# Kernel tuning notes

Hardware: AMD Instinct MI355X
Metric: run time of the kernel (lower is better)

The kernel has to match this reference:

```python
import jax, jax.numpy as jnp
import numpy as np

H = 768      # hidden_size
R = 16       # num_relations
NS = 64      # num_support
NQ = 128     # num_query
STEPS = 3    # propagation_steps


def setup_inputs() -> dict:
    key = jax.random.key(0)
    ks = jax.random.split(key, 16)
    s_h = 1.0 / np.sqrt(H)
    s_2h = 1.0 / np.sqrt(2 * H)
    f32 = jnp.float32
    return {
        'aspect_embeddings': jax.random.normal(ks[0], (NS, H), f32),
        'query_embeddings': jax.random.normal(ks[1], (NQ, H), f32),
        'support_labels': jax.random.randint(ks[2], (NS,), 0, 5),
        # similarity network: Linear(2H->H), ReLU, Linear(H->R), Softmax
        'W1s': (jax.random.normal(ks[3], (H, 2 * H), f32) * s_2h),
        'b1s': jnp.zeros((H,), f32),
        'W2s': (jax.random.normal(ks[4], (R, H), f32) * s_h),
        'b2s': jnp.zeros((R,), f32),
        # diversity network
        'W1d': (jax.random.normal(ks[5], (H, 2 * H), f32) * s_2h),
        'b1d': jnp.zeros((H,), f32),
        'W2d': (jax.random.normal(ks[6], (R, H), f32) * s_h),
        'b2d': jnp.zeros((R,), f32),
        # relation matrices [R, H, H] (scaled for numerical stability)
        'Rs': (jax.random.normal(ks[7], (R, H, H), f32) * s_h),
        'Rd': (jax.random.normal(ks[8], (R, H, H), f32) * s_h),
        # message MLP: Linear(H->H), ReLU, Linear(H->H)
        'Wm1': (jax.random.normal(ks[9], (H, H), f32) * s_h),
        'bm1': jnp.zeros((H,), f32),
        'Wm2': (jax.random.normal(ks[10], (H, H), f32) * s_h),
        'bm2': jnp.zeros((H,), f32),
        # GRUCell params (gate order: r, z, n as in torch)
        'Wih': (jax.random.normal(ks[11], (3 * H, H), f32) * s_h),
        'Whh': (jax.random.normal(ks[12], (3 * H, H), f32) * s_h),
        'bih': jnp.zeros((3 * H,), f32),
        'bhh': jnp.zeros((3 * H,), f32),
    }


def _relation_net(pf, W1, b1, W2, b2):
    # pf: [N, N, 2H] -> softmax weights [N, N, R]; dropout is identity (eval)
    hid = jax.nn.relu(jnp.einsum('ijk,hk->ijh', pf, W1) + b1)
    return jax.nn.softmax(jnp.einsum('ijh,rh->ijr', hid, W2) + b2, axis=-1)


def _drp_forward(aspect_embeddings, query_embeddings,
                 W1s, b1s, W2s, b2s, W1d, b1d, W2d, b2d,
                 Rs, Rd, Wm1, bm1, Wm2, bm2, Wih, Whh, bih, bhh):
    h = jnp.concatenate([aspect_embeddings, query_embeddings], axis=0)  # [N, H]
    N = h.shape[0]
    for _ in range(STEPS):
        # pairwise features [N, N, 2H]: (node_i, node_j)
        pf = jnp.concatenate([
            jnp.broadcast_to(h[:, None, :], (N, N, H)),
            jnp.broadcast_to(h[None, :, :], (N, N, H)),
        ], axis=-1)
        sw = _relation_net(pf, W1s, b1s, W2s, b2s)  # [N, N, R]
        dw = _relation_net(pf, W1d, b1d, W2d, b2d)  # [N, N, R]
        # relation-transformed embeddings: [N, R, H]
        ts = jnp.einsum('jh,rhd->jrd', h, Rs)
        td = jnp.einsum('jh,rhd->jrd', h, Rd)
        # relation-weighted messages: [N, N, H]
        msgs = jnp.einsum('ijr,jrd->ijd', sw, ts) + jnp.einsum('ijr,jrd->ijd', dw, td)
        pm = jax.nn.relu(msgs @ Wm1.T + bm1) @ Wm2.T + bm2  # [N, N, H]
        x = pm.mean(axis=1)  # aggregated message per node [N, H]
        # GRUCell update (torch gate order r, z, n)
        gx = x @ Wih.T + bih
        gh = h @ Whh.T + bhh
        r = jax.nn.sigmoid(gx[:, :H] + gh[:, :H])
        z = jax.nn.sigmoid(gx[:, H:2 * H] + gh[:, H:2 * H])
        n = jnp.tanh(gx[:, 2 * H:] + r * gh[:, 2 * H:])
        h = (1.0 - z) * n + z * h
    return h[NS:]  # updated query embeddings [NQ, H]


def reference(aspect_embeddings, support_labels, query_embeddings,
              W1s, b1s, W2s, b2s, W1d, b1d, W2d, b2d,
              Rs, Rd, Wm1, bm1, Wm2, bm2, Wih, Whh, bih, bhh):
    # support_labels is unused in the original forward
    return _drp_forward(aspect_embeddings, query_embeddings,
                        W1s, b1s, W2s, b2s, W1d, b1d, W2d, b2d,
                        Rs, Rd, Wm1, bm1, Wm2, bm2, Wih, Whh, bih, bhh)
```

## Files before the change

### kernel.cpp

```cpp
#include <hip/hip_runtime.h>
#include <hip/hip_bf16.h>

#define H 768
#define NTOT 192
#define A4W 3072
#define GW 2304

typedef __attribute__((ext_vector_type(4))) float f32x4;
typedef __attribute__((ext_vector_type(8))) unsigned short u16x8;
typedef __attribute__((ext_vector_type(4))) unsigned short u16x4;
typedef __attribute__((ext_vector_type(8))) __bf16 bf16x8v;

static __device__ __forceinline__ unsigned short f2bf(float f) {
  __hip_bfloat16 b = __float2bfloat16(f);
  return __builtin_bit_cast(unsigned short, b);
}
static __device__ __forceinline__ float bf2f(unsigned short u) {
  return __bfloat162float(__builtin_bit_cast(__hip_bfloat16, u));
}
static __device__ __forceinline__ f32x4 MFMA(u16x8 a, u16x8 b, f32x4 c) {
  return __builtin_amdgcn_mfma_f32_16x16x32_bf16(
      __builtin_bit_cast(bf16x8v, a), __builtin_bit_cast(bf16x8v, b), c, 0, 0, 0);
}
static __device__ __forceinline__ u16x8 ld8(const unsigned short* p) {
  return *(const u16x8*)p;
}
static __device__ __forceinline__ unsigned int cvtpk(float lo, float hi) {
  unsigned int r;
  asm("v_cvt_pk_bf16_f32 %0, %1, %2" : "=v"(r) : "v"(lo), "v"(hi));
  return r;
}
static __device__ __forceinline__ float relu(float x) { return fmaxf(x, 0.f); }

#define GLDS16(gp, lp)                                                   \
  __builtin_amdgcn_global_load_lds(                                      \
      (const __attribute__((address_space(1))) void*)(gp),               \
      (__attribute__((address_space(3))) void*)(lp), 16, 0, 0)

__global__ void k_prep(const float* __restrict__ Wm1, const float* __restrict__ W2s,
                       const float* __restrict__ W2d, const float* __restrict__ Whh,
                       const float* __restrict__ Wih, const float* __restrict__ Wm2,
                       const float* __restrict__ W1s, const float* __restrict__ W1d,
                       const float* __restrict__ b1s, const float* __restrict__ b1d,
                       const float* __restrict__ bm2, const float* __restrict__ bih,
                       const float* __restrict__ asp, const float* __restrict__ qry,
                       unsigned short* __restrict__ Wm1bf, unsigned short* __restrict__ W2sbf,
                       unsigned short* __restrict__ W2dbf, unsigned short* __restrict__ Whhh,
                       unsigned short* __restrict__ Whhl, unsigned short* __restrict__ Wm2th,
                       unsigned short* __restrict__ Wm2tl, unsigned short* __restrict__ W1cat,
                       float* __restrict__ b1cat, float* __restrict__ bc,
                       float* __restrict__ h, unsigned short* __restrict__ hhi,
                       unsigned short* __restrict__ hlo) {
  const int b = blockIdx.x, tid = threadIdx.x;
  if (b < 576) {
    int u = b * 256 + tid;
    float4 v = ((const float4*)Wm1)[u];
    u16x4 o; o[0] = f2bf(v.x); o[1] = f2bf(v.y); o[2] = f2bf(v.z); o[3] = f2bf(v.w);
    ((u16x4*)Wm1bf)[u] = o;
  } else if (b < 588) {
    int u = (b - 576) * 256 + tid;
    float4 v = ((const float4*)W2s)[u];
    u16x4 o; o[0] = f2bf(v.x); o[1] = f2bf(v.y); o[2] = f2bf(v.z); o[3] = f2bf(v.w);
    ((u16x4*)W2sbf)[u] = o;
  } else if (b < 600) {
    int u = (b - 588) * 256 + tid;
    float4 v = ((const float4*)W2d)[u];
    u16x4 o; o[0] = f2bf(v.x); o[1] = f2bf(v.y); o[2] = f2bf(v.z); o[3] = f2bf(v.w);
    ((u16x4*)W2dbf)[u] = o;
  } else if (b < 2328) {
    int u = (b - 600) * 256 + tid;
    float4 v = ((const float4*)Whh)[u];
    u16x4 oh, ol;
#pragma unroll
    for (int j = 0; j < 4; ++j) {
      float f = ((const float*)&v)[j];
      oh[j] = f2bf(f); ol[j] = f2bf(f - bf2f(oh[j]));
    }
    ((u16x4*)Whhh)[u] = oh; ((u16x4*)Whhl)[u] = ol;
  } else if (b < 2904) {
    int u = (b - 2328) * 256 + tid;
    float4 v = ((const float4*)Wm2)[u];
    int e_lin = u * 4;
    int er = e_lin / H, kc = e_lin - er * H;
#pragma unroll
    for (int j = 0; j < 4; ++j) {
      float f = ((const float*)&v)[j];
      unsigned short hi = f2bf(f);
      Wm2th[(size_t)(kc + j) * H + er] = hi;
      Wm2tl[(size_t)(kc + j) * H + er] = f2bf(f - bf2f(hi));
    }
  } else if (b < 5208) {
    int u = (b - 2904) * 256 + tid;
    int e = u * 4;
    int row = e / H, k = e - row * H;
    int part = row / H, o = row - part * H;
    const float* W = (part < 2) ? W1s : W1d;
    float4 v = *(const float4*)(W + (size_t)o * (2 * H) + (part & 1) * H + k);
    u16x4 ov; ov[0] = f2bf(v.x); ov[1] = f2bf(v.y); ov[2] = f2bf(v.z); ov[3] = f2bf(v.w);
    *(u16x4*)(W1cat + e) = ov;
    if (u < 768) {
      int e2 = u * 4, pp = e2 / H, oo = e2 - pp * H;
      float4 bv;
      if (pp == 0) bv = *(const float4*)(b1s + oo);
      else if (pp == 2) bv = *(const float4*)(b1d + oo);
      else bv = (float4){0.f, 0.f, 0.f, 0.f};
      *(float4*)(b1cat + e2) = bv;
    }
  } else if (b < 5784) {
    const int w = tid >> 6, l = tid & 63;
    const int gg = (b - 5208) * 4 + w;
    const float* row = Wih + (size_t)gg * H;
    float s = 0.f;
#pragma unroll
    for (int q = 0; q < 12; ++q) s += row[l + q * 64] * bm2[l + q * 64];
#pragma unroll
    for (int m = 32; m; m >>= 1) s += __shfl_xor(s, m);
    if (l == 0) bc[gg] = bih[gg] + s;
  } else {
    int u = (b - 5784) * 256 + tid;
    float4 v = (u < 12288) ? ((const float4*)asp)[u] : ((const float4*)qry)[u - 12288];
    ((float4*)h)[u] = v;
    u16x4 oh, ol;
#pragma unroll
    for (int j = 0; j < 4; ++j) {
      float f = ((const float*)&v)[j];
      oh[j] = f2bf(f); ol[j] = f2bf(f - bf2f(oh[j]));
    }
    ((u16x4*)hhi)[u] = oh; ((u16x4*)hlo)[u] = ol;
  }
}

__global__ __launch_bounds__(256) void k_pre2(const unsigned short* __restrict__ Wm1bf,
                                              const float* __restrict__ Rsf,
                                              const float* __restrict__ Rdf,
                                              unsigned short* __restrict__ RsWt,
                                              const float* __restrict__ Wih,
                                              const unsigned short* __restrict__ Bth,
                                              const unsigned short* __restrict__ Btl,
                                              unsigned short* __restrict__ Ch,
                                              unsigned short* __restrict__ Cl) {
  __shared__ unsigned short LDS[16384];
  const int wg = blockIdx.x;
  const int tid = threadIdx.x, w = tid >> 6, l = tid & 63;
  const int g = l >> 4, ln = l & 15;
  const int srow = l >> 3;
  const int skb = ((l & 7) ^ srow) * 8;
  const int x7 = ln & 7;

  if (wg >= 1152) {
    unsigned short* Ahl = LDS;
    unsigned short* All = LDS + 4096;
    unsigned short* Bhl = LDS + 8192;
    unsigned short* Bll = LDS + 12288;
    const int bid = wg - 1152;
    const int m0 = (bid / 12) * 64, n0 = (bid % 12) * 64;
    const unsigned short* Bgh = Bth + (size_t)(n0 + srow) * H + skb;
    const unsigned short* Bgl = Btl + (size_t)(n0 + srow) * H + skb;
    f32x4 acc[4];
#pragma unroll
    for (int mi = 0; mi < 4; ++mi) acc[mi] = (f32x4){0.f, 0.f, 0.f, 0.f};
    for (int kb = 0; kb < H; kb += 64) {
#pragma unroll
      for (int c2 = 0; c2 < 2; ++c2) {
        const int c = w * 2 + c2;
        GLDS16(Bgh + (size_t)(c * 8) * H + kb, &Bhl[c * 512]);
        GLDS16(Bgl + (size_t)(c * 8) * H + kb, &Bll[c * 512]);
      }
#pragma unroll
      for (int q = 0; q < 2; ++q) {
        const int idx = q * 256 + tid;
        const int row = idx >> 3, kb8 = idx & 7;
        const float* src = Wih + (size_t)(m0 + row) * H + kb + kb8 * 8;
        float4 v0 = *(const float4*)src;
        float4 v1 = *(const float4*)(src + 4);
        float fv[8] = {v0.x, v0.y, v0.z, v0.w, v1.x, v1.y, v1.z, v1.w};
        u16x8 oh, ol;
#pragma unroll
        for (int jq = 0; jq < 8; ++jq) {
          unsigned short hi = f2bf(fv[jq]);
          oh[jq] = hi;
          ol[jq] = f2bf(fv[jq] - bf2f(hi));
        }
        const int dst = row * 64 + (kb8 ^ (row & 7)) * 8;
        *(u16x8*)&Ahl[dst] = oh;
        *(u16x8*)&All[dst] = ol;
      }
      __syncthreads();
#pragma unroll
      for (int kk = 0; kk < 2; ++kk) {
        const int pb = ((kk * 4 + g) ^ x7) * 8;
        u16x8 bh = ld8(&Bhl[(w * 16 + ln) * 64 + pb]);
        u16x8 bl = ld8(&Bll[(w * 16 + ln) * 64 + pb]);
#pragma unroll
        for (int mi = 0; mi < 4; ++mi) {
          u16x8 ah = ld8(&Ahl[(mi * 16 + ln) * 64 + pb]);
          u16x8 al = ld8(&All[(mi * 16 + ln) * 64 + pb]);
          acc[mi] = MFMA(ah, bh, acc[mi]);
          acc[mi] = MFMA(ah, bl, acc[mi]);
          acc[mi] = MFMA(al, bh, acc[mi]);
        }
      }
      __syncthreads();
    }
#pragma unroll
    for (int mi = 0; mi < 4; ++mi) {
      const int col = n0 + w * 16 + ln;
#pragma unroll
      for (int pp = 0; pp < 4; ++pp) {
        const int row = m0 + mi * 16 + g * 4 + pp;
        const float val = acc[mi][pp];
        unsigned short hi = f2bf(val);
        Ch[(size_t)row * H + col] = hi;
        Cl[(size_t)row * H + col] = f2bf(val - bf2f(hi));
      }
    }
    return;
  }

  unsigned short* Asl = LDS;
  unsigned short* Bsl = LDS + 8192;
  const int nb = (wg & 7) * 144 + (wg >> 3);
  const int z = nb / 36, t5 = nb - z * 36;
  const int d0 = (t5 / 6) * 128, k0 = (t5 % 6) * 128;
  const int wr = w >> 1, wc = w & 1;
  const unsigned short* Ag = Wm1bf + (size_t)(d0 + srow) * H + skb;
  const float* Bg = ((z < 16) ? Rsf : Rdf) + (size_t)(z & 15) * (H * H);
  f32x4 acc[4][4];
#pragma unroll
  for (int mi = 0; mi < 4; ++mi)
#pragma unroll
    for (int ni = 0; ni < 4; ++ni) acc[mi][ni] = (f32x4){0.f, 0.f, 0.f, 0.f};
  for (int kb = 0; kb < H; kb += 64) {
#pragma unroll
    for (int c4 = 0; c4 < 4; ++c4) {
      const int c = w * 4 + c4;
      GLDS16(Ag + (size_t)(c * 8) * H + kb, &Asl[c * 512]);
    }
#pragma unroll
    for (int q = 0; q < 4; ++q) {
      const int idx = q * 256 + tid;
      const int row = idx >> 3, kb8 = idx & 7;
      const float* src = Bg + (size_t)(k0 + row) * H + kb + kb8 * 8;
      float4 v0 = *(const float4*)src;
      float4 v1 = *(const float4*)(src + 4);
      u16x8 o;
      unsigned int* po = (unsigned int*)&o;
      po[0] = cvtpk(v0.x, v0.y);
      po[1] = cvtpk(v0.z, v0.w);
      po[2] = cvtpk(v1.x, v1.y);
      po[3] = cvtpk(v1.z, v1.w);
      *(u16x8*)&Bsl[row * 64 + (kb8 ^ (row & 7)) * 8] = o;
    }
    __syncthreads();
#pragma unroll
    for (int kk = 0; kk < 2; ++kk) {
      u16x8 af[4], bf[4];
      const int pb = ((kk * 4 + g) ^ x7) * 8;
#pragma unroll
      for (int mi = 0; mi < 4; ++mi) af[mi] = ld8(&Asl[(wr * 64 + mi * 16 + ln) * 64 + pb]);
#pragma unroll
      for (int ni = 0; ni < 4; ++ni) bf[ni] = ld8(&Bsl[(wc * 64 + ni * 16 + ln) * 64 + pb]);
#pragma unroll
      for (int mi = 0; mi < 4; ++mi)
#pragma unroll
        for (int ni = 0; ni < 4; ++ni) acc[mi][ni] = MFMA(af[mi], bf[ni], acc[mi][ni]);
    }
    __syncthreads();
  }
#pragma unroll
  for (int mi = 0; mi < 4; ++mi) {
    const int d = d0 + wr * 64 + mi * 16 + g * 4;
#pragma unroll
    for (int ni = 0; ni < 4; ++ni) {
      const int k = k0 + wc * 64 + ni * 16 + ln;
      unsigned short* o = RsWt + ((size_t)d * 32 + z) * H + k;
#pragma unroll
      for (int pp = 0; pp < 4; ++pp) o[(size_t)pp * 32 * H] = f2bf(acc[mi][ni][pp]);
    }
  }
}

__global__ __launch_bounds__(256) void k_btks(
    const unsigned short* __restrict__ Ahi, const unsigned short* __restrict__ Alo,
    const unsigned short* __restrict__ Bhi, const unsigned short* __restrict__ Blo,
    float* __restrict__ Cp) {
  const int tid = threadIdx.x;
  const int w = tid >> 6, l = tid & 63, g = l >> 4, ln = l & 15;
  const int m0 = blockIdx.y * 64 + w * 16;
  const int n0 = blockIdx.x * 64;
  const int kh = blockIdx.z, kb0 = kh * 192;
  const unsigned short* aph = Ahi + (size_t)(m0 + ln) * H + kb0 + g * 8;
  const unsigned short* apl = Alo + (size_t)(m0 + ln) * H + kb0 + g * 8;
  const unsigned short* bph[4];
  const unsigned short* bpl[4];
#pragma unroll
  for (int nt = 0; nt < 4; ++nt) {
    bph[nt] = Bhi + (size_t)(n0 + nt * 16 + ln) * H + kb0 + g * 8;
    bpl[nt] = Blo + (size_t)(n0 + nt * 16 + ln) * H + kb0 + g * 8;
  }
  f32x4 acc[4];
#pragma unroll
  for (int nt = 0; nt < 4; ++nt) acc[nt] = (f32x4){0.f, 0.f, 0.f, 0.f};
  u16x8 ah[2], al[2], bh[2][4], bl[2][4];
  ah[0] = ld8(aph);
  al[0] = ld8(apl);
#pragma unroll
  for (int nt = 0; nt < 4; ++nt) { bh[0][nt] = ld8(bph[nt]); bl[0][nt] = ld8(bpl[nt]); }
#pragma unroll
  for (int t = 0; t < 6; ++t) {
    const int cur = t & 1, nxt = cur ^ 1;
    if (t < 5) {
      const int ko = (t + 1) * 32;
      ah[nxt] = ld8(aph + ko);
      al[nxt] = ld8(apl + ko);
#pragma unroll
      for (int nt = 0; nt < 4; ++nt) {
        bh[nxt][nt] = ld8(bph[nt] + ko);
        bl[nxt][nt] = ld8(bpl[nt] + ko);
      }
    }
#pragma unroll
    for (int nt = 0; nt < 4; ++nt) {
      acc[nt] = MFMA(ah[cur], bh[cur][nt], acc[nt]);
      acc[nt] = MFMA(ah[cur], bl[cur][nt], acc[nt]);
      acc[nt] = MFMA(al[cur], bh[cur][nt], acc[nt]);
    }
  }
#pragma unroll
  for (int nt = 0; nt < 4; ++nt) {
    const int col = n0 + nt * 16 + ln;
#pragma unroll
    for (int pp = 0; pp < 4; ++pp) {
      const int row = m0 + g * 4 + pp;
      Cp[(size_t)kh * (NTOT * GW) + (size_t)row * GW + col] = acc[nt][pp];
    }
  }
}

__global__ __launch_bounds__(256) void k_tile(
    const unsigned short* __restrict__ hhi, const unsigned short* __restrict__ hlo,
    const unsigned short* __restrict__ W1cat, const float* __restrict__ b1cat,
    const unsigned short* __restrict__ Whhh, const unsigned short* __restrict__ Whhl,
    const float* __restrict__ bhh, const unsigned short* __restrict__ RsWt,
    float* __restrict__ A4, float* __restrict__ ghb, unsigned short* __restrict__ twB) {
  __shared__ unsigned short Ah[4096], Al[4096], Bh[8192], Bl[8192];
  const int bid = blockIdx.x;
  const int tid = threadIdx.x, w = tid >> 6, l = tid & 63, g = l >> 4, ln = l & 15;
  int path, m, n;
  if (bid < 54)       { path = 0; n = bid / 3;         m = bid % 3; }
  else if (bid < 126) { path = 1; n = (bid - 54) / 3;  m = (bid - 54) % 3; }
  else                { path = 2; n = (bid - 126) / 3; m = (bid - 126) % 3; }
  const int m0 = m * 64, n0 = n * 128;
  const bool isgh = (path == 0);
  const unsigned short* Bsrc = (path == 0) ? Whhh : (path == 1) ? W1cat : RsWt;
  const int srow = l >> 3;
  const int skb = ((l & 7) ^ srow) * 8;
  const unsigned short* Agh = hhi + (size_t)(m0 + srow) * H + skb;
  const unsigned short* Agl = hlo + (size_t)(m0 + srow) * H + skb;
  const unsigned short* Bgh = Bsrc + (size_t)(n0 + srow) * H + skb;
  const unsigned short* Bgl = Whhl + (size_t)((isgh ? n0 : 0) + srow) * H + skb;
  f32x4 acc[4][2];
#pragma unroll
  for (int mi = 0; mi < 4; ++mi)
#pragma unroll
    for (int ni = 0; ni < 2; ++ni) acc[mi][ni] = (f32x4){0.f, 0.f, 0.f, 0.f};
  const int x7 = ln & 7;
  for (int kb = 0; kb < H; kb += 64) {
#pragma unroll
    for (int c2 = 0; c2 < 2; ++c2) {
      const int c = w * 2 + c2;
      GLDS16(Agh + (size_t)(c * 8) * H + kb, &Ah[c * 512]);
      if (isgh) GLDS16(Agl + (size_t)(c * 8) * H + kb, &Al[c * 512]);
    }
#pragma unroll
    for (int c4 = 0; c4 < 4; ++c4) {
      const int c = w * 4 + c4;
      GLDS16(Bgh + (size_t)(c * 8) * H + kb, &Bh[c * 512]);
      if (isgh) GLDS16(Bgl + (size_t)(c * 8) * H + kb, &Bl[c * 512]);
    }
    __syncthreads();
#pragma unroll
    for (int kk = 0; kk < 2; ++kk) {
      const int pb = ((kk * 4 + g) ^ x7) * 8;
      u16x8 af[4], bf[2];
#pragma unroll
      for (int mi = 0; mi < 4; ++mi) af[mi] = ld8(&Ah[(mi * 16 + ln) * 64 + pb]);
#pragma unroll
      for (int ni = 0; ni < 2; ++ni) bf[ni] = ld8(&Bh[(w * 32 + ni * 16 + ln) * 64 + pb]);
      if (isgh) {
        u16x8 alf[4], blf[2];
#pragma unroll
        for (int mi = 0; mi < 4; ++mi) alf[mi] = ld8(&Al[(mi * 16 + ln) * 64 + pb]);
#pragma unroll
        for (int ni = 0; ni < 2; ++ni) blf[ni] = ld8(&Bl[(w * 32 + ni * 16 + ln) * 64 + pb]);
#pragma unroll
        for (int mi = 0; mi < 4; ++mi)
#pragma unroll
          for (int ni = 0; ni < 2; ++ni) {
            acc[mi][ni] = MFMA(af[mi], bf[ni], acc[mi][ni]);
            acc[mi][ni] = MFMA(af[mi], blf[ni], acc[mi][ni]);
            acc[mi][ni] = MFMA(alf[mi], bf[ni], acc[mi][ni]);
          }
      } else {
#pragma unroll
        for (int mi = 0; mi < 4; ++mi)
#pragma unroll
          for (int ni = 0; ni < 2; ++ni) acc[mi][ni] = MFMA(af[mi], bf[ni], acc[mi][ni]);
      }
    }
    __syncthreads();
  }
  if (path == 2) {
#pragma unroll
    for (int mi = 0; mi < 4; ++mi)
#pragma unroll
      for (int ni = 0; ni < 2; ++ni) {
        const int c = n0 + w * 32 + ni * 16 + ln;
#pragma unroll
        for (int pp = 0; pp < 4; ++pp) {
          const int j = m0 + mi * 16 + g * 4 + pp;
          twB[(size_t)j * 24576 + c] = f2bf(acc[mi][ni][pp]);
        }
      }
  } else {
    const int N = isgh ? GW : A4W;
    float* C = isgh ? ghb : A4;
    const float* bias = isgh ? bhh : b1cat;
#pragma unroll
    for (int mi = 0; mi < 4; ++mi)
#pragma unroll
      for (int ni = 0; ni < 2; ++ni) {
        const int col = n0 + w * 32 + ni * 16 + ln;
        const float bv = bias[col];
#pragma unroll
        for (int pp = 0; pp < 4; ++pp) {
          const int row = m0 + mi * 16 + g * 4 + pp;
          C[(size_t)row * N + col] = acc[mi][ni][pp] + bv;
        }
      }
  }
}

__global__ __launch_bounds__(256) void k_pairlog(
    const float* __restrict__ A4, const unsigned short* __restrict__ W2sbf,
    const unsigned short* __restrict__ W2dbf, const float* __restrict__ b2s,
    const float* __restrict__ b2d, unsigned short* __restrict__ swA) {
  __shared__ float red[8][16][17];
  const int i = blockIdx.x, jb = blockIdx.y;
  const int tid = threadIdx.x, w = tid >> 6, l = tid & 63;
  const int g = l >> 4, ln = l & 15;
  const int j = jb * 16 + ln;
  const float* BsP = A4 + (size_t)j * A4W + 768 + g * 8;
  const float* BdP = A4 + (size_t)j * A4W + 2304 + g * 8;
  const float* AsP = A4 + (size_t)i * A4W + g * 8;
  const float* AdP = A4 + (size_t)i * A4W + 1536 + g * 8;
  const unsigned short* WsP = W2sbf + (size_t)ln * H + g * 8;
  const unsigned short* WdP = W2dbf + (size_t)ln * H + g * 8;
  f32x4 accs = (f32x4){0.f, 0.f, 0.f, 0.f}, accd = (f32x4){0.f, 0.f, 0.f, 0.f};
#pragma unroll
  for (int tt = 0; tt < 6; ++tt) {
    const int ko = (w * 6 + tt) * 32;
    float4 b0 = *(const float4*)(BsP + ko), b1 = *(const float4*)(BsP + ko + 4);
    float4 a0 = *(const float4*)(AsP + ko), a1 = *(const float4*)(AsP + ko + 4);
    float4 e0 = *(const float4*)(BdP + ko), e1 = *(const float4*)(BdP + ko + 4);
    float4 c0 = *(const float4*)(AdP + ko), c1 = *(const float4*)(AdP + ko + 4);
    u16x8 afs, afd;
    unsigned int* ps = (unsigned int*)&afs;
    ps[0] = cvtpk(relu(a0.x + b0.x), relu(a0.y + b0.y));
    ps[1] = cvtpk(relu(a0.z + b0.z), relu(a0.w + b0.w));
    ps[2] = cvtpk(relu(a1.x + b1.x), relu(a1.y + b1.y));
    ps[3] = cvtpk(relu(a1.z + b1.z), relu(a1.w + b1.w));
    unsigned int* pd = (unsigned int*)&afd;
    pd[0] = cvtpk(relu(c0.x + e0.x), relu(c0.y + e0.y));
    pd[1] = cvtpk(relu(c0.z + e0.z), relu(c0.w + e0.w));
    pd[2] = cvtpk(relu(c1.x + e1.x), relu(c1.y + e1.y));
    pd[3] = cvtpk(relu(c1.z + e1.z), relu(c1.w + e1.w));
    accs = MFMA(afs, ld8(WsP + ko), accs);
    accd = MFMA(afd, ld8(WdP + ko), accd);
  }
#pragma unroll
  for (int pp = 0; pp < 4; ++pp) {
    red[w * 2][g * 4 + pp][ln] = accs[pp];
    red[w * 2 + 1][g * 4 + pp][ln] = accd[pp];
  }
  __syncthreads();
  const int j2 = tid >> 4, r = tid & 15;
  float vs = red[0][j2][r] + red[2][j2][r] + red[4][j2][r] + red[6][j2][r] + b2s[r];
  float vd = red[1][j2][r] + red[3][j2][r] + red[5][j2][r] + red[7][j2][r] + b2d[r];
  float ms = vs;
  ms = fmaxf(ms, __shfl_xor(ms, 1)); ms = fmaxf(ms, __shfl_xor(ms, 2));
  ms = fmaxf(ms, __shfl_xor(ms, 4)); ms = fmaxf(ms, __shfl_xor(ms, 8));
  float md = vd;
  md = fmaxf(md, __shfl_xor(md, 1)); md = fmaxf(md, __shfl_xor(md, 2));
  md = fmaxf(md, __shfl_xor(md, 4)); md = fmaxf(md, __shfl_xor(md, 8));
  float es = __expf(vs - ms), ed = __expf(vd - md);
  float ss = es;
  ss += __shfl_xor(ss, 1); ss += __shfl_xor(ss, 2); ss += __shfl_xor(ss, 4); ss += __shfl_xor(ss, 8);
  float sd = ed;
  sd += __shfl_xor(sd, 1); sd += __shfl_xor(sd, 2); sd += __shfl_xor(sd, 4); sd += __shfl_xor(sd, 8);
  const size_t o = (size_t)(jb * 16 + j2) * 6144 + (size_t)i * 32;
  swA[o + r] = f2bf(es / ss);
  swA[o + 16 + r] = f2bf(ed / sd);
}

__global__ __launch_bounds__(256) void k_pairmsg(const unsigned short* __restrict__ swA,
                                                 const unsigned short* __restrict__ twB,
                                                 const float* __restrict__ bm1,
                                                 float* __restrict__ vpart) {
  const int dt = blockIdx.x, it = blockIdx.y, js = blockIdx.z;
  const int tid = threadIdx.x;
  const int w = tid >> 6, l = tid & 63, g = l >> 4, ln = l & 15;
  const int i0 = it * 64 + w * 16;
  const int d0 = dt * 64;
  float bm1v[4];
#pragma unroll
  for (int nt = 0; nt < 4; ++nt) bm1v[nt] = bm1[d0 + nt * 16 + ln];
  f32x4 vacc[4];
#pragma unroll
  for (int nt = 0; nt < 4; ++nt) vacc[nt] = (f32x4){0.f, 0.f, 0.f, 0.f};
  const unsigned short* ap = swA + (size_t)(i0 + ln) * 32 + g * 8 + (size_t)js * 24 * 6144;
  const unsigned short* bp[4];
#pragma unroll
  for (int nt = 0; nt < 4; ++nt)
    bp[nt] = twB + (size_t)(d0 + nt * 16 + ln) * 32 + g * 8 + (size_t)js * 24 * 24576;
  const f32x4 z4 = (f32x4){0.f, 0.f, 0.f, 0.f};
#pragma unroll 4
  for (int jj = 0; jj < 24; ++jj) {
    u16x8 a = ld8(ap + (size_t)jj * 6144);
#pragma unroll
    for (int nt = 0; nt < 4; ++nt) {
      u16x8 b = ld8(bp[nt] + (size_t)jj * 24576);
      f32x4 mf = MFMA(a, b, z4);
#pragma unroll
      for (int pp = 0; pp < 4; ++pp) vacc[nt][pp] += fmaxf(mf[pp] + bm1v[nt], 0.f);
    }
  }
#pragma unroll
  for (int nt = 0; nt < 4; ++nt)
#pragma unroll
    for (int pp = 0; pp < 4; ++pp) {
      const int row = i0 + g * 4 + pp;
      vpart[(size_t)js * 147456 + (size_t)row * H + d0 + nt * 16 + ln] = vacc[nt][pp];
    }
}

__global__ void k_vred(const float* __restrict__ vpart, unsigned short* __restrict__ vhi,
                       unsigned short* __restrict__ vlo) {
  int e = blockIdx.x * 256 + threadIdx.x;
  float s = 0.f;
#pragma unroll
  for (int q = 0; q < 8; ++q) s += vpart[(size_t)q * 147456 + e];
  s *= (1.0f / 192.0f);
  unsigned short hi = f2bf(s);
  vhi[e] = hi;
  vlo[e] = f2bf(s - bf2f(hi));
}

__global__ void k_gru(const float* __restrict__ gxp, const float* __restrict__ bcv,
                      const float* __restrict__ gh, float* __restrict__ h,
                      unsigned short* __restrict__ hhi, unsigned short* __restrict__ hlo,
                      float* __restrict__ out, int last) {
  int e = blockIdx.x * 256 + threadIdx.x;
  int i = e / H, k = e - i * H;
  size_t base = (size_t)i * GW;
  const size_t S = (size_t)NTOT * GW;
  float rr = gxp[base + k] + gxp[S + base + k] + gxp[2 * S + base + k] +
             gxp[3 * S + base + k] + bcv[k] + gh[base + k];
  float zz = gxp[base + H + k] + gxp[S + base + H + k] + gxp[2 * S + base + H + k] +
             gxp[3 * S + base + H + k] + bcv[H + k] + gh[base + H + k];
  float r = 1.f / (1.f + __expf(-rr));
  float z = 1.f / (1.f + __expf(-zz));
  float nn = gxp[base + 2 * H + k] + gxp[S + base + 2 * H + k] +
             gxp[2 * S + base + 2 * H + k] + gxp[3 * S + base + 2 * H + k] +
             bcv[2 * H + k];
  float n = tanhf(nn + r * gh[base + 2 * H + k]);
  float hv = (1.f - z) * n + z * h[e];
  h[e] = hv;
  unsigned short hi = f2bf(hv);
  hhi[e] = hi;
  hlo[e] = f2bf(hv - bf2f(hi));
  if (last && i >= 64) out[(size_t)(i - 64) * H + k] = hv;
}


extern "C" void kernel_launch(void* const* d_in, const int* in_sizes, int n_in,
                              void* d_out, int out_size, void* d_ws, size_t ws_size,
                              hipStream_t stream) {
  const float* asp = (const float*)d_in[0];
  const float* qry = (const float*)d_in[1];
  const float* W1s = (const float*)d_in[3];
  const float* b1s = (const float*)d_in[4];
  const float* W2s = (const float*)d_in[5];
  const float* b2s = (const float*)d_in[6];
  const float* W1d = (const float*)d_in[7];
  const float* b1d = (const float*)d_in[8];
  const float* W2d = (const float*)d_in[9];
  const float* b2d = (const float*)d_in[10];
  const float* Rs  = (const float*)d_in[11];
  const float* Rd  = (const float*)d_in[12];
  const float* Wm1 = (const float*)d_in[13];
  const float* bm1 = (const float*)d_in[14];
  const float* Wm2 = (const float*)d_in[15];
  const float* bm2 = (const float*)d_in[16];
  const float* Wih = (const float*)d_in[17];
  const float* Whh = (const float*)d_in[18];
  const float* bih = (const float*)d_in[19];
  const float* bhh = (const float*)d_in[20];
  float* out = (float*)d_out;

  char* p = (char*)d_ws;
  auto take = [&](size_t bytes) {
    char* q = p;
    p += (bytes + 255) & ~(size_t)255;
    return q;
  };
  float* h            = (float*)take((size_t)NTOT * H * 4);
  unsigned short* hhi = (unsigned short*)take((size_t)NTOT * H * 2);
  unsigned short* hlo = (unsigned short*)take((size_t)NTOT * H * 2);
  float* A4           = (float*)take((size_t)NTOT * A4W * 4);
  float* ghb          = (float*)take((size_t)NTOT * GW * 4);
  unsigned short* vhi = (unsigned short*)take((size_t)NTOT * H * 2);
  unsigned short* vlo = (unsigned short*)take((size_t)NTOT * H * 2);
  float* vpart        = (float*)take((size_t)8 * NTOT * H * 4);
  unsigned short* swA = (unsigned short*)take((size_t)NTOT * NTOT * 32 * 2);
  unsigned short* twB = (unsigned short*)take((size_t)NTOT * H * 32 * 2);
  unsigned short* RsWt = (unsigned short*)take((size_t)2 * 16 * H * H * 2);
  unsigned short* Wm1bf = (unsigned short*)take((size_t)H * H * 2);
  unsigned short* W2sbf = (unsigned short*)take((size_t)16 * H * 2);
  unsigned short* W2dbf = (unsigned short*)take((size_t)16 * H * 2);
  unsigned short* W1cat = (unsigned short*)take((size_t)A4W * H * 2);
  float* b1cat        = (float*)take((size_t)A4W * 4);
  unsigned short* Whhh = (unsigned short*)take((size_t)GW * H * 2);
  unsigned short* Whhl = (unsigned short*)take((size_t)GW * H * 2);
  unsigned short* Wch  = (unsigned short*)take((size_t)GW * H * 2);
  unsigned short* Wcl  = (unsigned short*)take((size_t)GW * H * 2);
  float* bc           = (float*)take((size_t)GW * 4);
  unsigned short* Wm2th = (unsigned short*)((char*)d_ws + 1179648);
  unsigned short* Wm2tl = Wm2th + (size_t)H * H;

  k_prep<<<5928, 256, 0, stream>>>(Wm1, W2s, W2d, Whh, Wih, Wm2, W1s, W1d, b1s, b1d,
                                   bm2, bih, asp, qry,
                                   Wm1bf, W2sbf, W2dbf, Whhh, Whhl,
                                   Wm2th, Wm2tl, W1cat, b1cat, bc, h, hhi, hlo);
  k_pre2<<<1584, 256, 0, stream>>>(Wm1bf, Rs, Rd, RsWt, Wih, Wm2th, Wm2tl, Wch, Wcl);

  for (int step = 0; step < 3; ++step) {
    k_tile<<<702, 256, 0, stream>>>(hhi, hlo, W1cat, b1cat, Whhh, Whhl, bhh, RsWt,
                                    A4, ghb, twB);
    k_pairlog<<<dim3(192, 12), 256, 0, stream>>>(A4, W2sbf, W2dbf, b2s, b2d, swA);
    k_pairmsg<<<dim3(12, 3, 8), 256, 0, stream>>>(swA, twB, bm1, vpart);
    k_vred<<<576, 256, 0, stream>>>(vpart, vhi, vlo);
    k_btks<<<dim3(36, 3, 4), 256, 0, stream>>>(vhi, vlo, Wch, Wcl, (float*)twB);
    k_gru<<<576, 256, 0, stream>>>((float*)twB, bc, ghb, h, hhi, hlo, out, step == 2);
  }
  (void)in_sizes; (void)n_in; (void)out_size; (void)ws_size;
}
```

Before: 493.7 us.

## Register-prefetch next B tile in relation-weight GEMM and remap k_tile blocks by XCD

The Wm1×R precompute GEMM now loads the next k-step's fp32 B tile into registers before running the MFMAs on the current tile. It converts and stores that tile to LDS after a barrier, so global-load latency overlaps with compute. This raises register pressure and adds a second barrier per iteration. Separately, k_tile remaps blockIdx so that consecutive logical blocks land on the same XCD, which is meant to improve L2 locality for shared operands.

```diff
diff --git a/kernel.cpp b/kernel.cpp
--- a/kernel.cpp
+++ b/kernel.cpp
@@ -225,33 +225,44 @@
   const int wr = w >> 1, wc = w & 1;
   const unsigned short* Ag = Wm1bf + (size_t)(d0 + srow) * H + skb;
   const float* Bg = ((z < 16) ? Rsf : Rdf) + (size_t)(z & 15) * (H * H);
+  const int kb8 = tid & 7, rb = tid >> 3;
+  const float* Bq = Bg + (size_t)(k0 + rb) * H + kb8 * 8;
+  const int bdst = rb * 64 + (kb8 ^ (rb & 7)) * 8;
+
+#define LOADB_(kbv, Ra, Rb)                                  \
+  _Pragma("unroll") for (int q = 0; q < 4; ++q) {            \
+    const float* s_ = Bq + (size_t)(q * 32) * H + (kbv);     \
+    Ra[q] = *(const float4*)s_;                              \
+    Rb[q] = *(const float4*)(s_ + 4);                        \
+  }
+#define WRITEB_(Ra, Rb)                                      \
+  _Pragma("unroll") for (int q = 0; q < 4; ++q) {            \
+    u16x8 o_; unsigned int* po_ = (unsigned int*)&o_;        \
+    po_[0] = cvtpk(Ra[q].x, Ra[q].y);                        \
+    po_[1] = cvtpk(Ra[q].z, Ra[q].w);                        \
+    po_[2] = cvtpk(Rb[q].x, Rb[q].y);                        \
+    po_[3] = cvtpk(Rb[q].z, Rb[q].w);                        \
+    *(u16x8*)&Bsl[q * 2048 + bdst] = o_;                     \
+  }
+#define GLDSA_(kbv)                                          \
+  _Pragma("unroll") for (int c4 = 0; c4 < 4; ++c4) {         \
+    const int c_ = w * 4 + c4;                               \
+    GLDS16(Ag + (size_t)(c_ * 8) * H + (kbv), &Asl[c_ * 512]); \
+  }
+
   f32x4 acc[4][4];
 #pragma unroll
   for (int mi = 0; mi < 4; ++mi)
 #pragma unroll
     for (int ni = 0; ni < 4; ++ni) acc[mi][ni] = (f32x4){0.f, 0.f, 0.f, 0.f};
-  for (int kb = 0; kb < H; kb += 64) {
-#pragma unroll
-    for (int c4 = 0; c4 < 4; ++c4) {
-      const int c = w * 4 + c4;
-      GLDS16(Ag + (size_t)(c * 8) * H + kb, &Asl[c * 512]);
-    }
-#pragma unroll
-    for (int q = 0; q < 4; ++q) {
-      const int idx = q * 256 + tid;
-      const int row = idx >> 3, kb8 = idx & 7;
-      const float* src = Bg + (size_t)(k0 + row) * H + kb + kb8 * 8;
-      float4 v0 = *(const float4*)src;
-      float4 v1 = *(const float4*)(src + 4);
-      u16x8 o;
-      unsigned int* po = (unsigned int*)&o;
-      po[0] = cvtpk(v0.x, v0.y);
-      po[1] = cvtpk(v0.z, v0.w);
-      po[2] = cvtpk(v1.x, v1.y);
-      po[3] = cvtpk(v1.z, v1.w);
-      *(u16x8*)&Bsl[row * 64 + (kb8 ^ (row & 7)) * 8] = o;
-    }
-    __syncthreads();
+  float4 ra[4], rbv[4];
+  LOADB_(0, ra, rbv);
+  GLDSA_(0);
+  WRITEB_(ra, rbv);
+  __syncthreads();
+#pragma unroll
+  for (int t = 0; t < 12; ++t) {
+    if (t < 11) { LOADB_((t + 1) * 64, ra, rbv); }
 #pragma unroll
     for (int kk = 0; kk < 2; ++kk) {
       u16x8 af[4], bf[4];
@@ -266,6 +277,11 @@
         for (int ni = 0; ni < 4; ++ni) acc[mi][ni] = MFMA(af[mi], bf[ni], acc[mi][ni]);
     }
     __syncthreads();
+    if (t < 11) {
+      WRITEB_(ra, rbv);
+      GLDSA_((t + 1) * 64);
+      __syncthreads();
+    }
   }
 #pragma unroll
   for (int mi = 0; mi < 4; ++mi) {
@@ -278,6 +294,9 @@
       for (int pp = 0; pp < 4; ++pp) o[(size_t)pp * 32 * H] = f2bf(acc[mi][ni][pp]);
     }
   }
+#undef LOADB_
+#undef WRITEB_
+#undef GLDSA_
 }
 
 __global__ __launch_bounds__(256) void k_btks(
@@ -344,7 +363,10 @@
     const float* __restrict__ bhh, const unsigned short* __restrict__ RsWt,
     float* __restrict__ A4, float* __restrict__ ghb, unsigned short* __restrict__ twB) {
   __shared__ unsigned short Ah[4096], Al[4096], Bh[8192], Bl[8192];
-  const int bid = blockIdx.x;
+  const int orig = blockIdx.x;
+  const int qq = 87, rr = 6;
+  const int xcd = orig & 7, idx = orig >> 3;
+  const int bid = (xcd < rr ? xcd * (qq + 1) : rr * (qq + 1) + (xcd - rr) * qq) + idx;
   const int tid = threadIdx.x, w = tid >> 6, l = tid & 63, g = l >> 4, ln = l & 15;
   int path, m, n;
   if (bid < 54)       { path = 0; n = bid / 3;         m = bid % 3; }
```

Result: faster. 479.3 us (-2.9%).
